# Performance work log

Hardware: AMD Instinct MI355X
Metric: run time of the kernel (lower is better)

## Reference

```python
import jax, jax.numpy as jnp
import numpy as np

H = 2048          # hidden_size
NH = 16           # num heads
DN = 128          # nope_head_dim
DR = 64           # rope_head_dim
DQ = DN + DR      # q_head_dim = 192
DV = 128          # v_head_dim
KVR = 512         # kv_lora_rank
QR = 1536         # q_lora_rank
THETA = 100000.0
EPS = 1e-5


def rms_norm(x, w, eps=EPS):
    var = jnp.mean(x * x, axis=-1, keepdims=True)
    return w * (x * jax.lax.rsqrt(var + eps))


def rotate_half(x):
    x1, x2 = jnp.split(x, 2, axis=-1)
    return jnp.concatenate([-x2, x1], axis=-1)


def rope_cos_sin(seq_len, dim, base, dtype):
    inv_freq = 1.0 / (base ** (jnp.arange(0, dim, 2, dtype=jnp.float32) / dim))
    t = jnp.arange(seq_len, dtype=jnp.float32)
    freqs = jnp.outer(t, inv_freq)          # [S, dim/2]
    emb = jnp.concatenate([freqs, freqs], axis=-1)  # [S, dim]
    return jnp.cos(emb).astype(dtype), jnp.sin(emb).astype(dtype)


def setup_inputs() -> dict:
    key = jax.random.key(0)
    ks = jax.random.split(key, 9)
    B, S = 1, 2048
    sc = lambda fan_in: 1.0 / np.sqrt(fan_in)
    return {
        "x":           jax.random.normal(ks[0], (B, S, H), jnp.float32),
        "wq_down":     jax.random.normal(ks[1], (H, QR), jnp.float32) * sc(H),
        "q_up_norm_w": jnp.ones((QR,), jnp.float32),
        "wq_up":       jax.random.normal(ks[2], (QR, NH * DQ), jnp.float32) * sc(QR),
        "wkv_down":    jax.random.normal(ks[3], (H, KVR), jnp.float32) * sc(H),
        "kv_norm_w":   jnp.ones((KVR,), jnp.float32),
        "wk_up":       jax.random.normal(ks[4], (KVR, NH * DQ), jnp.float32) * sc(KVR),
        "wv_up":       jax.random.normal(ks[5], (KVR, NH * DV), jnp.float32) * sc(KVR),
        "wo":          jax.random.normal(ks[6], (NH * DV, H), jnp.float32) * sc(NH * DV),
    }


def reference(x, wq_down, q_up_norm_w, wq_up, wkv_down, kv_norm_w, wk_up, wv_up, wo):
    B, S, _ = x.shape
    # low-rank Q path
    q_lat = rms_norm(x @ wq_down, q_up_norm_w)
    q = (q_lat @ wq_up).reshape(B, S, NH, DQ)
    q_nope, q_pe = q[..., :DN], q[..., DN:]
    # low-rank KV path
    kv_lat = rms_norm(x @ wkv_down, kv_norm_w)
    k = (kv_lat @ wk_up).reshape(B, S, NH, DQ)
    v = (kv_lat @ wv_up).reshape(B, S, NH, DV)
    k_nope, k_pe = k[..., :DN], k[..., DN:]
    # partial RoPE on the rope dims ([B,S,NH,DR]; cos/sin broadcast over B,NH)
    cos, sin = rope_cos_sin(S, DR, THETA, x.dtype)
    cos = cos[None, :, None, :]
    sin = sin[None, :, None, :]
    q_pe = q_pe * cos + rotate_half(q_pe) * sin
    k_pe = k_pe * cos + rotate_half(k_pe) * sin
    q = jnp.concatenate([q_nope, q_pe], axis=-1)  # [B,S,NH,DQ]
    k = jnp.concatenate([k_nope, k_pe], axis=-1)
    # causal SDPA, scale = 1/sqrt(q_head_dim)
    scale = 1.0 / np.sqrt(DQ)
    scores = jnp.einsum("bqhd,bkhd->bhqk", q, k) * scale
    causal = jnp.tril(jnp.ones((S, S), dtype=bool))
    scores = jnp.where(causal[None, None], scores, jnp.finfo(scores.dtype).min)
    probs = jax.nn.softmax(scores, axis=-1)
    out = jnp.einsum("bhqk,bkhd->bqhd", probs, v).reshape(B, S, NH * DV)
    return out @ wo
```

## Files before the change

kernel.cpp:

```cpp
#include <hip/hip_runtime.h>
#include <math.h>

typedef unsigned short u16;
typedef short s16x8 __attribute__((ext_vector_type(8)));
typedef __bf16 bf16x8 __attribute__((ext_vector_type(8)));
typedef float f32x4 __attribute__((ext_vector_type(4)));

#define S_LEN 2048
#define NHEAD 16
#define QCOLS 3072
#define VCOLS 2048
#define ATT_SCALE 0.07216878364870323f

__device__ __forceinline__ u16 f2bf(float f) {
    unsigned u = __float_as_uint(f);
    u += 0x7fffu + ((u >> 16) & 1u);
    return (u16)(u >> 16);
}
__device__ __forceinline__ float bf2f(u16 h) {
    return __uint_as_float(((unsigned)h) << 16);
}

typedef const __attribute__((address_space(1))) void gas_void;
typedef __attribute__((address_space(3))) void las_void;
__device__ __forceinline__ void gload_lds16(const void* g, void* l) {
    __builtin_amdgcn_global_load_lds(
        (gas_void*)(unsigned long long)g,
        (las_void*)(unsigned)(unsigned long long)l, 16, 0, 0);
}

template<int BM, int BN, int OMODE>
__global__ __launch_bounds__(256) void gemm_bf16(
    const u16* __restrict__ A, const u16* __restrict__ Bt,
    void* __restrict__ Cv, int M, int N, int K,
    const float* __restrict__ cost, const float* __restrict__ sint)
{
    constexpr int BK = 64;
    __shared__ u16 As[2][BM * BK];
    __shared__ u16 Bs[2][BN * BK];
    const int t = threadIdx.x;
    const int lane = t & 63, wid = t >> 6;
    const int wr = wid >> 1, wc = wid & 1;
    const int g = lane >> 4, cl = lane & 15;
    const size_t bm = (size_t)blockIdx.y * BM;
    const size_t bn = (size_t)blockIdx.x * BN;
    constexpr int MR = BM / 32, NR = BN / 32;
    constexpr int APW = BM * BK * 2 / 1024 / 4;
    constexpr int BPW = BN * BK * 2 / 1024 / 4;

    auto stage = [&](int buf, int k0) {
#pragma unroll
        for (int i = 0; i < APW; ++i) {
            int rnd = wid * APW + i;
            int fb  = (rnd << 10) + (lane << 4);
            int row = fb >> 7;
            int ke  = (fb & 127) >> 1;
            gload_lds16(A + (bm + row) * K + k0 + ke, (char*)As[buf] + (rnd << 10));
        }
#pragma unroll
        for (int i = 0; i < BPW; ++i) {
            int rnd = wid * BPW + i;
            int fb  = (rnd << 10) + (lane << 4);
            int row = fb >> 7;
            int ke  = (fb & 127) >> 1;
            gload_lds16(Bt + (bn + row) * K + k0 + ke, (char*)Bs[buf] + (rnd << 10));
        }
    };

    f32x4 acc[MR][NR] = {};
    stage(0, 0);
    int cur = 0;
    for (int k0 = 0; k0 < K; k0 += BK) {
        __syncthreads();
        if (k0 + BK < K) stage(cur ^ 1, k0 + BK);
#pragma unroll
        for (int ks = 0; ks < 2; ++ks) {
            s16x8 av[MR], bv[NR];
#pragma unroll
            for (int m = 0; m < MR; ++m)
                av[m] = *(const s16x8*)((const char*)As[cur] +
                        (wr*(BM/2) + m*16 + cl) * 128 + ks*64 + g*16);
#pragma unroll
            for (int n = 0; n < NR; ++n)
                bv[n] = *(const s16x8*)((const char*)Bs[cur] +
                        (wc*(BN/2) + n*16 + cl) * 128 + ks*64 + g*16);
#pragma unroll
            for (int m = 0; m < MR; ++m)
#pragma unroll
                for (int n = 0; n < NR; ++n)
                    acc[m][n] = __builtin_amdgcn_mfma_f32_16x16x32_bf16(
                        __builtin_bit_cast(bf16x8, av[m]),
                        __builtin_bit_cast(bf16x8, bv[n]), acc[m][n], 0, 0, 0);
        }
        cur ^= 1;
    }

    if constexpr (OMODE == 3) {
        const int band = ((int)(bn >> 6)) + wc;
        const bool pe = (band % 3) == 2;
        u16* C = (u16*)Cv;
#pragma unroll
        for (int m = 0; m < MR; ++m) {
            const size_t rbase = bm + wr*(BM/2) + m*16 + g*4;
            if (pe) {
#pragma unroll
                for (int n = 0; n < 2; ++n) {
                    const int j = n*16 + cl;
                    const size_t colA = bn + wc*(BN/2) + n*16 + cl;
#pragma unroll
                    for (int jj = 0; jj < 4; ++jj) {
                        const size_t r = rbase + jj;
                        float co = cost[r*32 + j], sn = sint[r*32 + j];
                        float a = acc[m][n][jj], b = acc[m][n+2][jj];
                        C[r*N + colA]      = f2bf(a*co - b*sn);
                        C[r*N + colA + 32] = f2bf(b*co + a*sn);
                    }
                }
            } else {
#pragma unroll
                for (int n = 0; n < NR; ++n) {
                    const size_t col = bn + wc*(BN/2) + n*16 + cl;
#pragma unroll
                    for (int jj = 0; jj < 4; ++jj)
                        C[(rbase + jj)*N + col] = f2bf(acc[m][n][jj]);
                }
            }
        }
    } else {
#pragma unroll
        for (int m = 0; m < MR; ++m)
#pragma unroll
            for (int n = 0; n < NR; ++n) {
                size_t col = bn + wc*(BN/2) + n*16 + cl;
#pragma unroll
                for (int j = 0; j < 4; ++j) {
                    size_t row = bm + wr*(BM/2) + m*16 + g*4 + j;
                    if constexpr (OMODE == 0)
                        ((float*)Cv)[row * N + col] = acc[m][n][j];
                    else if constexpr (OMODE == 1)
                        ((u16*)Cv)[row * N + col] = f2bf(acc[m][n][j]);
                    else
                        ((u16*)Cv)[col * M + row] = f2bf(acc[m][n][j]);
                }
            }
    }
}

__global__ __launch_bounds__(256) void transpose_cast5(
    const float* __restrict__ w0, u16* __restrict__ o0,
    const float* __restrict__ w1, u16* __restrict__ o1,
    const float* __restrict__ w2, u16* __restrict__ o2,
    const float* __restrict__ w3, u16* __restrict__ o3,
    const float* __restrict__ w4, u16* __restrict__ o4)
{
    const int z = blockIdx.z;
    const float* in; u16* out; int K, N;
    if      (z == 0) { in = w0; out = o0; K = 2048; N = 1536; }
    else if (z == 1) { in = w1; out = o1; K = 2048; N = 512;  }
    else if (z == 2) { in = w2; out = o2; K = 1536; N = 3072; }
    else if (z == 3) { in = w3; out = o3; K = 512;  N = 3072; }
    else             { in = w4; out = o4; K = 512;  N = 2048; }
    const int bn = blockIdx.x * 32, bk = blockIdx.y * 32;
    if (bn >= N || bk >= K) return;

    __shared__ float tile[32][33];
    const int tx = threadIdx.x & 31, ty = threadIdx.x >> 5;
#pragma unroll
    for (int r = 0; r < 32; r += 8)
        tile[ty + r][tx] = in[(size_t)(bk + ty + r) * N + bn + tx];
    __syncthreads();
#pragma unroll
    for (int r = 0; r < 32; r += 8)
        out[(size_t)(bn + ty + r) * K + bk + tx] = f2bf(tile[tx][ty + r]);
}

__global__ __launch_bounds__(256) void transpose_cast(
    const float* __restrict__ in, u16* __restrict__ out, int K, int N)
{
    __shared__ float tile[32][33];
    const int bk = blockIdx.y * 32, bn = blockIdx.x * 32;
    const int tx = threadIdx.x & 31, ty = threadIdx.x >> 5;
#pragma unroll
    for (int r = 0; r < 32; r += 8)
        tile[ty + r][tx] = in[(size_t)(bk + ty + r) * N + bn + tx];
    __syncthreads();
#pragma unroll
    for (int r = 0; r < 32; r += 8)
        out[(size_t)(bn + ty + r) * K + bk + tx] = f2bf(tile[tx][ty + r]);
}

__global__ __launch_bounds__(256) void cast_f32_bf16(
    const float* __restrict__ in, u16* __restrict__ out, long n)
{
    long i = ((long)blockIdx.x * 256 + threadIdx.x) * 4;
    if (i >= n) return;
    f32x4 v = *(const f32x4*)(in + i);
    ushort4 q;
    q.x = f2bf(v[0]); q.y = f2bf(v[1]); q.z = f2bf(v[2]); q.w = f2bf(v[3]);
    *(ushort4*)(out + i) = q;
}

__global__ __launch_bounds__(256) void rmsnorm_bf(
    const float* __restrict__ x, const float* __restrict__ w,
    u16* __restrict__ o, int N, float invN)
{
    const int row = blockIdx.x;
    const float* xr = x + (size_t)row * N;
    u16* orow = o + (size_t)row * N;
    const int t = threadIdx.x;
    float ss = 0.f;
    for (int i = t * 4; i < N; i += 1024) {
        f32x4 v = *(const f32x4*)&xr[i];
        ss += v[0]*v[0] + v[1]*v[1] + v[2]*v[2] + v[3]*v[3];
    }
#pragma unroll
    for (int off = 32; off > 0; off >>= 1) ss += __shfl_down(ss, off, 64);
    __shared__ float red[4];
    __shared__ float sinv;
    if ((t & 63) == 0) red[t >> 6] = ss;
    __syncthreads();
    if (t == 0) sinv = rsqrtf((red[0]+red[1]+red[2]+red[3]) * invN + 1e-5f);
    __syncthreads();
    const float si = sinv;
    for (int i = t * 4; i < N; i += 1024) {
        f32x4 v = *(const f32x4*)&xr[i];
        f32x4 wv = *(const f32x4*)&w[i];
        ushort4 q;
        q.x = f2bf(v[0]*wv[0]*si); q.y = f2bf(v[1]*wv[1]*si);
        q.z = f2bf(v[2]*wv[2]*si); q.w = f2bf(v[3]*wv[3]*si);
        *(ushort4*)&orow[i] = q;
    }
}

__global__ __launch_bounds__(256) void rope_table_k(
    float* __restrict__ cost, float* __restrict__ sint)
{
    int idx = blockIdx.x * 256 + threadIdx.x;
    int tp = idx >> 5, j = idx & 31;
    float invf = powf(100000.0f, -(float)j * (1.0f / 32.0f));
    float fr = (float)tp * invf;
    cost[idx] = cosf(fr);
    sint[idx] = sinf(fr);
}

__global__ __launch_bounds__(256) void attn_mfma(
    const u16* __restrict__ qg, const u16* __restrict__ kg,
    const u16* __restrict__ vtg, u16* __restrict__ og)
{
    __shared__ u16 Ks[64 * 192];
    __shared__ u16 VTs[128 * 64];
    __shared__ u16 Ps[4][16 * 64];

    const int t = threadIdx.x, lane = t & 63, wid = t >> 6;
    const int g = lane >> 4, cl = lane & 15;
    const int h = blockIdx.y;
    const int bx = blockIdx.x;
    const int qt = (bx & 1) ? (31 - (bx >> 1)) : (bx >> 1);
    const int qbase = qt * 64;
    const int wrow = wid * 16;

    s16x8 qv[6];
    {
        const u16* qrow = qg + (size_t)(qbase + wrow + cl) * QCOLS + h * 192;
#pragma unroll
        for (int s = 0; s < 6; ++s)
            qv[s] = *(const s16x8*)(qrow + s * 32 + g * 8);
    }
    float mreg[4], lreg[4];
#pragma unroll
    for (int j = 0; j < 4; ++j) { mreg[j] = -1e30f; lreg[j] = 0.f; }

    f32x4 accO[8] = {};
    char* pw = (char*)Ps[wid];

    for (int kt = 0; kt <= qt; ++kt) {
        const int kbase = kt * 64;
        __syncthreads();
        {
            const char* ksrc = (const char*)(kg + (size_t)kbase * QCOLS + h * 192);
#pragma unroll
            for (int i = 0; i < 6; ++i) {
                int rnd = wid * 6 + i;
                int fb  = (rnd << 10) + (lane << 4);
                int row = fb / 384;
                int cb  = fb - row * 384;
                gload_lds16(ksrc + (size_t)row * (QCOLS * 2)
                                 + (cb ^ ((row & 7) << 4)),
                            (char*)Ks + (rnd << 10));
            }
            const char* vsrc = (const char*)(vtg + (size_t)(h * 128) * S_LEN + kbase);
#pragma unroll
            for (int i = 0; i < 4; ++i) {
                int rnd = wid * 4 + i;
                int fb  = (rnd << 10) + (lane << 4);
                int dv  = fb >> 7;
                int cb  = fb & 127;
                gload_lds16(vsrc + (size_t)dv * (S_LEN * 2)
                                 + (cb ^ ((dv & 7) << 4)),
                            (char*)VTs + (rnd << 10));
            }
        }
        __syncthreads();

        f32x4 accS[4] = {};
        __builtin_amdgcn_s_setprio(1);
#pragma unroll
        for (int n = 0; n < 4; ++n) {
            const int kvrow = n * 16 + cl;
            const char* krow = (const char*)Ks + kvrow * 384;
            const int sw = (kvrow & 7) << 4;
#pragma unroll
            for (int s = 0; s < 6; ++s) {
                s16x8 kv8 = *(const s16x8*)(krow + ((s * 64 + g * 16) ^ sw));
                accS[n] = __builtin_amdgcn_mfma_f32_16x16x32_bf16(
                    __builtin_bit_cast(bf16x8, qv[s]),
                    __builtin_bit_cast(bf16x8, kv8), accS[n], 0, 0, 0);
            }
        }
        __builtin_amdgcn_s_setprio(0);

        float pm[4][4];
        float cj[4];
#pragma unroll
        for (int j = 0; j < 4; ++j) {
            const int qrow = qbase + wrow + g * 4 + j;
            float mx = -1e30f;
#pragma unroll
            for (int n = 0; n < 4; ++n) {
                int kcol = kbase + n * 16 + cl;
                float s = accS[n][j] * ATT_SCALE;
                s = (kcol <= qrow) ? s : -1e30f;
                pm[n][j] = s;
                mx = fmaxf(mx, s);
            }
#pragma unroll
            for (int off = 1; off < 16; off <<= 1)
                mx = fmaxf(mx, __shfl_xor(mx, off, 64));
            float mnew = fmaxf(mreg[j], mx);
            float c = __expf(mreg[j] - mnew);
            float rs = 0.f;
#pragma unroll
            for (int n = 0; n < 4; ++n) {
                float p = __expf(pm[n][j] - mnew);
                pm[n][j] = p;
                rs += p;
            }
#pragma unroll
            for (int off = 1; off < 16; off <<= 1)
                rs += __shfl_xor(rs, off, 64);
            lreg[j] = lreg[j] * c + rs;
            mreg[j] = mnew;
            cj[j] = c;
        }

#pragma unroll
        for (int n = 0; n < 4; ++n)
#pragma unroll
            for (int j = 0; j < 4; ++j) {
                int q = g * 4 + j;
                int byte = (q * 128 + (n * 16 + cl) * 2) ^ ((q & 7) << 4);
                *(u16*)(pw + byte) = f2bf(pm[n][j]);
            }

#pragma unroll
        for (int nb = 0; nb < 8; ++nb)
#pragma unroll
            for (int j = 0; j < 4; ++j) accO[nb][j] *= cj[j];

        __builtin_amdgcn_s_setprio(1);
#pragma unroll
        for (int ks = 0; ks < 2; ++ks) {
            s16x8 pa = *(const s16x8*)(pw +
                ((cl * 128 + ks * 64 + g * 16) ^ ((cl & 7) << 4)));
#pragma unroll
            for (int nb = 0; nb < 8; ++nb) {
                s16x8 vb = *(const s16x8*)((const char*)VTs +
                    (((nb * 16 + cl) * 128 + ks * 64 + g * 16) ^ ((cl & 7) << 4)));
                accO[nb] = __builtin_amdgcn_mfma_f32_16x16x32_bf16(
                    __builtin_bit_cast(bf16x8, pa),
                    __builtin_bit_cast(bf16x8, vb), accO[nb], 0, 0, 0);
            }
        }
        __builtin_amdgcn_s_setprio(0);
    }

#pragma unroll
    for (int j = 0; j < 4; ++j) {
        float inv = 1.f / lreg[j];
        u16* orow = og + (size_t)(qbase + wrow + g * 4 + j) * VCOLS + h * 128;
#pragma unroll
        for (int nb = 0; nb < 8; ++nb)
            orow[nb * 16 + cl] = f2bf(accO[nb][j] * inv);
    }
}

extern "C" void kernel_launch(void* const* d_in, const int* in_sizes, int n_in,
                              void* d_out, int out_size, void* d_ws, size_t ws_size,
                              hipStream_t stream)
{
    const float* x         = (const float*)d_in[0];
    const float* wq_down   = (const float*)d_in[1];
    const float* q_norm_w  = (const float*)d_in[2];
    const float* wq_up     = (const float*)d_in[3];
    const float* wkv_down  = (const float*)d_in[4];
    const float* kv_norm_w = (const float*)d_in[5];
    const float* wk_up     = (const float*)d_in[6];
    const float* wv_up     = (const float*)d_in[7];
    const float* wo        = (const float*)d_in[8];
    float* out = (float*)d_out;
    char* ws = (char*)d_ws;

    u16*  WQD_T  = (u16*)(ws + 0);
    u16*  WKVD_T = (u16*)(ws + 6291456);
    u16*  WQU_T  = (u16*)(ws + 8388608);
    u16*  WKU_T  = (u16*)(ws + 17825792);
    u16*  WVU_T  = (u16*)(ws + 20971520);
    u16*  XBF    = (u16*)(ws + 23068672);
    float* QLAT  = (float*)(ws + 31457280);
    float* KVLAT = (float*)(ws + 44040192);
    u16*  QLATB  = (u16*)(ws + 48234496);
    u16*  KVLATB = (u16*)(ws + 54525952);
    u16*  QBUF   = (u16*)(ws + 56623104);
    u16*  KBUF   = (u16*)(ws + 69206016);
    float* COST  = (float*)(ws + 81788928);
    float* SINT  = (float*)(ws + 82051072);
    u16*  WO_T   = (u16*)(ws + 0);
    u16*  VTBUF  = (u16*)(ws + 31457280);
    u16*  ATTNO  = (u16*)(ws + 23068672);

    transpose_cast5<<<dim3(96, 64, 5), 256, 0, stream>>>(
        wq_down, WQD_T, wkv_down, WKVD_T, wq_up, WQU_T, wk_up, WKU_T, wv_up, WVU_T);
    cast_f32_bf16<<<4096, 256, 0, stream>>>(x, XBF, (long)S_LEN * 2048);
    rope_table_k<<<256, 256, 0, stream>>>(COST, SINT);

    gemm_bf16<128,128,0><<<dim3(12, 16), 256, 0, stream>>>(
        XBF, WQD_T,  QLAT,  2048, 1536, 2048, nullptr, nullptr);
    gemm_bf16< 64, 64,0><<<dim3( 8, 32), 256, 0, stream>>>(
        XBF, WKVD_T, KVLAT, 2048,  512, 2048, nullptr, nullptr);
    rmsnorm_bf<<<2048, 256, 0, stream>>>(QLAT,  q_norm_w,  QLATB,  1536, 1.f/1536.f);
    rmsnorm_bf<<<2048, 256, 0, stream>>>(KVLAT, kv_norm_w, KVLATB, 512,  1.f/512.f);
    transpose_cast<<<dim3(64, 64), 256, 0, stream>>>(wo, WO_T, 2048, 2048);

    gemm_bf16<128,128,3><<<dim3(24, 16), 256, 0, stream>>>(
        QLATB,  WQU_T, QBUF,  2048, 3072, 1536, COST, SINT);
    gemm_bf16<128,128,3><<<dim3(24, 16), 256, 0, stream>>>(
        KVLATB, WKU_T, KBUF,  2048, 3072, 512,  COST, SINT);
    gemm_bf16<128,128,2><<<dim3(16, 16), 256, 0, stream>>>(
        KVLATB, WVU_T, VTBUF, 2048, 2048, 512,  nullptr, nullptr);

    attn_mfma<<<dim3(32, 16), 256, 0, stream>>>(QBUF, KBUF, VTBUF, ATTNO);
    gemm_bf16<128,128,0><<<dim3(16, 16), 256, 0, stream>>>(
        ATTNO, WO_T, out, 2048, 2048, 2048, nullptr, nullptr);
}
```

Baseline: 375.2 us.

## Fuse K/V up-projections, bf16 latent rmsnorm, register-prefetched attention K/V

The down-projection GEMMs now write bf16 latents directly, and a single combined rmsnorm kernel normalizes both buffers in place. This replaces the fp32 intermediates and the two separate norm launches. The K and V up-projections merge into one GEMM over a contiguous WKU/WVU weight block with N=5120, and blocks past column 3072 write V transposed. The attention kernel swaps the async global-to-LDS loads for register prefetch of the next K/V tile, overlapped with compute. It also transposes the score MFMA so each lane owns one query row, which simplifies the softmax reductions, at the cost of extra syncs and register pressure plus bf16 rounding of the latents before the norm.

```diff
diff --git a/kernel.cpp b/kernel.cpp
--- a/kernel.cpp
+++ b/kernel.cpp
@@ -2,6 +2,7 @@
 #include <math.h>
 
 typedef unsigned short u16;
+typedef short s16x4 __attribute__((ext_vector_type(4)));
 typedef short s16x8 __attribute__((ext_vector_type(8)));
 typedef __bf16 bf16x8 __attribute__((ext_vector_type(8)));
 typedef float f32x4 __attribute__((ext_vector_type(4)));
@@ -33,7 +34,8 @@
 __global__ __launch_bounds__(256) void gemm_bf16(
     const u16* __restrict__ A, const u16* __restrict__ Bt,
     void* __restrict__ Cv, int M, int N, int K,
-    const float* __restrict__ cost, const float* __restrict__ sint)
+    const float* __restrict__ cost, const float* __restrict__ sint,
+    u16* __restrict__ Cv2)
 {
     constexpr int BK = 64;
     __shared__ u16 As[2][BM * BK];
@@ -95,34 +97,49 @@
         cur ^= 1;
     }
 
-    if constexpr (OMODE == 3) {
+    if constexpr (OMODE == 3 || OMODE == 4) {
         const int band = ((int)(bn >> 6)) + wc;
-        const bool pe = (band % 3) == 2;
         u16* C = (u16*)Cv;
-#pragma unroll
-        for (int m = 0; m < MR; ++m) {
-            const size_t rbase = bm + wr*(BM/2) + m*16 + g*4;
-            if (pe) {
-#pragma unroll
-                for (int n = 0; n < 2; ++n) {
-                    const int j = n*16 + cl;
-                    const size_t colA = bn + wc*(BN/2) + n*16 + cl;
-#pragma unroll
-                    for (int jj = 0; jj < 4; ++jj) {
-                        const size_t r = rbase + jj;
-                        float co = cost[r*32 + j], sn = sint[r*32 + j];
-                        float a = acc[m][n][jj], b = acc[m][n+2][jj];
-                        C[r*N + colA]      = f2bf(a*co - b*sn);
-                        C[r*N + colA + 32] = f2bf(b*co + a*sn);
+        if (OMODE == 4 && band >= 48) {
+#pragma unroll
+            for (int m = 0; m < MR; ++m)
+#pragma unroll
+                for (int n = 0; n < NR; ++n) {
+                    size_t vcol = bn + wc*(BN/2) + n*16 + cl - 3072;
+#pragma unroll
+                    for (int j = 0; j < 4; ++j) {
+                        size_t row = bm + wr*(BM/2) + m*16 + g*4 + j;
+                        Cv2[vcol * M + row] = f2bf(acc[m][n][j]);
                     }
                 }
-            } else {
-#pragma unroll
-                for (int n = 0; n < NR; ++n) {
-                    const size_t col = bn + wc*(BN/2) + n*16 + cl;
-#pragma unroll
-                    for (int jj = 0; jj < 4; ++jj)
-                        C[(rbase + jj)*N + col] = f2bf(acc[m][n][jj]);
+        } else {
+            const bool pe = (band % 3) == 2;
+            const int NN = 3072;
+#pragma unroll
+            for (int m = 0; m < MR; ++m) {
+                const size_t rbase = bm + wr*(BM/2) + m*16 + g*4;
+                if (pe) {
+#pragma unroll
+                    for (int n = 0; n < 2; ++n) {
+                        const int j = n*16 + cl;
+                        const size_t colA = bn + wc*(BN/2) + n*16 + cl;
+#pragma unroll
+                        for (int jj = 0; jj < 4; ++jj) {
+                            const size_t r = rbase + jj;
+                            float co = cost[r*32 + j], sn = sint[r*32 + j];
+                            float a = acc[m][n][jj], b = acc[m][n+2][jj];
+                            C[r*NN + colA]      = f2bf(a*co - b*sn);
+                            C[r*NN + colA + 32] = f2bf(b*co + a*sn);
+                        }
+                    }
+                } else {
+#pragma unroll
+                    for (int n = 0; n < NR; ++n) {
+                        const size_t col = bn + wc*(BN/2) + n*16 + cl;
+#pragma unroll
+                        for (int jj = 0; jj < 4; ++jj)
+                            C[(rbase + jj)*NN + col] = f2bf(acc[m][n][jj]);
+                    }
                 }
             }
         }
@@ -200,18 +217,21 @@
     *(ushort4*)(out + i) = q;
 }
 
-__global__ __launch_bounds__(256) void rmsnorm_bf(
-    const float* __restrict__ x, const float* __restrict__ w,
-    u16* __restrict__ o, int N, float invN)
-{
-    const int row = blockIdx.x;
-    const float* xr = x + (size_t)row * N;
-    u16* orow = o + (size_t)row * N;
+__global__ __launch_bounds__(256) void rmsnorm2(
+    u16* __restrict__ qb, const float* __restrict__ qw,
+    u16* __restrict__ kvb, const float* __restrict__ kvw)
+{
+    const int r = blockIdx.x;
+    u16* buf; const float* w; int N; float invN;
+    if (r < 2048) { buf = qb + (size_t)r * 1536; w = qw; N = 1536; invN = 1.f/1536.f; }
+    else { buf = kvb + (size_t)(r - 2048) * 512; w = kvw; N = 512; invN = 1.f/512.f; }
     const int t = threadIdx.x;
+
     float ss = 0.f;
-    for (int i = t * 4; i < N; i += 1024) {
-        f32x4 v = *(const f32x4*)&xr[i];
-        ss += v[0]*v[0] + v[1]*v[1] + v[2]*v[2] + v[3]*v[3];
+    for (int i = t * 8; i < N; i += 2048) {
+        s16x8 v = *(const s16x8*)&buf[i];
+#pragma unroll
+        for (int e = 0; e < 8; ++e) { float f = bf2f((u16)v[e]); ss += f * f; }
     }
 #pragma unroll
     for (int off = 32; off > 0; off >>= 1) ss += __shfl_down(ss, off, 64);
@@ -222,13 +242,13 @@
     if (t == 0) sinv = rsqrtf((red[0]+red[1]+red[2]+red[3]) * invN + 1e-5f);
     __syncthreads();
     const float si = sinv;
-    for (int i = t * 4; i < N; i += 1024) {
-        f32x4 v = *(const f32x4*)&xr[i];
-        f32x4 wv = *(const f32x4*)&w[i];
-        ushort4 q;
-        q.x = f2bf(v[0]*wv[0]*si); q.y = f2bf(v[1]*wv[1]*si);
-        q.z = f2bf(v[2]*wv[2]*si); q.w = f2bf(v[3]*wv[3]*si);
-        *(ushort4*)&orow[i] = q;
+    for (int i = t * 8; i < N; i += 2048) {
+        s16x8 v = *(const s16x8*)&buf[i];
+        s16x8 o;
+#pragma unroll
+        for (int e = 0; e < 8; ++e)
+            o[e] = (short)f2bf(bf2f((u16)v[e]) * w[i + e] * si);
+        *(s16x8*)&buf[i] = o;
     }
 }
 
@@ -266,41 +286,53 @@
         for (int s = 0; s < 6; ++s)
             qv[s] = *(const s16x8*)(qrow + s * 32 + g * 8);
     }
-    float mreg[4], lreg[4];
-#pragma unroll
-    for (int j = 0; j < 4; ++j) { mreg[j] = -1e30f; lreg[j] = 0.f; }
-
+
+    float mreg = -1e30f, lreg = 0.f;
     f32x4 accO[8] = {};
     char* pw = (char*)Ps[wid];
 
+    s16x8 kreg[6], vreg[4];
+    const char* kh = (const char*)(kg + (size_t)h * 192);
+    const char* vh = (const char*)(vtg + (size_t)(h * 128) * S_LEN);
+
+    auto loadKV = [&](int kt2) {
+        const char* ksrc = kh + (size_t)(kt2 * 64) * (QCOLS * 2);
+#pragma unroll
+        for (int i = 0; i < 6; ++i) {
+            int fb = i * 4096 + t * 16;
+            int row = fb / 384, cb = fb - row * 384;
+            kreg[i] = *(const s16x8*)(ksrc + (size_t)row * (QCOLS * 2) + cb);
+        }
+        const char* vsrc = vh + (size_t)(kt2 * 64) * 2;
+#pragma unroll
+        for (int i = 0; i < 4; ++i) {
+            int fb = i * 4096 + t * 16;
+            int dv = fb >> 7, cb = fb & 127;
+            vreg[i] = *(const s16x8*)(vsrc + (size_t)dv * (S_LEN * 2) + cb);
+        }
+    };
+    auto writeKV = [&]() {
+#pragma unroll
+        for (int i = 0; i < 6; ++i) {
+            int fb = i * 4096 + t * 16;
+            int row = fb / 384, cb = fb - row * 384;
+            *(s16x8*)((char*)Ks + row * 384 + (cb ^ ((row & 7) << 4))) = kreg[i];
+        }
+#pragma unroll
+        for (int i = 0; i < 4; ++i) {
+            int fb = i * 4096 + t * 16;
+            int dv = fb >> 7, cb = fb & 127;
+            *(s16x8*)((char*)VTs + dv * 128 + (cb ^ ((dv & 7) << 4))) = vreg[i];
+        }
+    };
+
+    loadKV(0);
+    writeKV();
+    __syncthreads();
+
     for (int kt = 0; kt <= qt; ++kt) {
         const int kbase = kt * 64;
-        __syncthreads();
-        {
-            const char* ksrc = (const char*)(kg + (size_t)kbase * QCOLS + h * 192);
-#pragma unroll
-            for (int i = 0; i < 6; ++i) {
-                int rnd = wid * 6 + i;
-                int fb  = (rnd << 10) + (lane << 4);
-                int row = fb / 384;
-                int cb  = fb - row * 384;
-                gload_lds16(ksrc + (size_t)row * (QCOLS * 2)
-                                 + (cb ^ ((row & 7) << 4)),
-                            (char*)Ks + (rnd << 10));
-            }
-            const char* vsrc = (const char*)(vtg + (size_t)(h * 128) * S_LEN + kbase);
-#pragma unroll
-            for (int i = 0; i < 4; ++i) {
-                int rnd = wid * 4 + i;
-                int fb  = (rnd << 10) + (lane << 4);
-                int dv  = fb >> 7;
-                int cb  = fb & 127;
-                gload_lds16(vsrc + (size_t)dv * (S_LEN * 2)
-                                 + (cb ^ ((dv & 7) << 4)),
-                            (char*)VTs + (rnd << 10));
-            }
-        }
-        __syncthreads();
+        if (kt < qt) loadKV(kt + 1);
 
         f32x4 accS[4] = {};
         __builtin_amdgcn_s_setprio(1);
@@ -313,55 +345,55 @@
             for (int s = 0; s < 6; ++s) {
                 s16x8 kv8 = *(const s16x8*)(krow + ((s * 64 + g * 16) ^ sw));
                 accS[n] = __builtin_amdgcn_mfma_f32_16x16x32_bf16(
-                    __builtin_bit_cast(bf16x8, qv[s]),
-                    __builtin_bit_cast(bf16x8, kv8), accS[n], 0, 0, 0);
+                    __builtin_bit_cast(bf16x8, kv8),
+                    __builtin_bit_cast(bf16x8, qv[s]), accS[n], 0, 0, 0);
             }
         }
         __builtin_amdgcn_s_setprio(0);
 
+        const int qrow_g = qbase + wrow + cl;
         float pm[4][4];
-        float cj[4];
-#pragma unroll
-        for (int j = 0; j < 4; ++j) {
-            const int qrow = qbase + wrow + g * 4 + j;
-            float mx = -1e30f;
-#pragma unroll
-            for (int n = 0; n < 4; ++n) {
-                int kcol = kbase + n * 16 + cl;
+        float mx = -1e30f;
+#pragma unroll
+        for (int n = 0; n < 4; ++n)
+#pragma unroll
+            for (int j = 0; j < 4; ++j) {
+                int kcol = kbase + n * 16 + g * 4 + j;
                 float s = accS[n][j] * ATT_SCALE;
-                s = (kcol <= qrow) ? s : -1e30f;
+                s = (kcol <= qrow_g) ? s : -1e30f;
                 pm[n][j] = s;
                 mx = fmaxf(mx, s);
             }
-#pragma unroll
-            for (int off = 1; off < 16; off <<= 1)
-                mx = fmaxf(mx, __shfl_xor(mx, off, 64));
-            float mnew = fmaxf(mreg[j], mx);
-            float c = __expf(mreg[j] - mnew);
-            float rs = 0.f;
-#pragma unroll
-            for (int n = 0; n < 4; ++n) {
+        mx = fmaxf(mx, __shfl_xor(mx, 16, 64));
+        mx = fmaxf(mx, __shfl_xor(mx, 32, 64));
+        float mnew = fmaxf(mreg, mx);
+        float c = __expf(mreg - mnew);
+        float rs = 0.f;
+#pragma unroll
+        for (int n = 0; n < 4; ++n)
+#pragma unroll
+            for (int j = 0; j < 4; ++j) {
                 float p = __expf(pm[n][j] - mnew);
                 pm[n][j] = p;
                 rs += p;
             }
-#pragma unroll
-            for (int off = 1; off < 16; off <<= 1)
-                rs += __shfl_xor(rs, off, 64);
-            lreg[j] = lreg[j] * c + rs;
-            mreg[j] = mnew;
-            cj[j] = c;
-        }
-
-#pragma unroll
-        for (int n = 0; n < 4; ++n)
-#pragma unroll
-            for (int j = 0; j < 4; ++j) {
-                int q = g * 4 + j;
-                int byte = (q * 128 + (n * 16 + cl) * 2) ^ ((q & 7) << 4);
-                *(u16*)(pw + byte) = f2bf(pm[n][j]);
-            }
-
+        rs += __shfl_xor(rs, 16, 64);
+        rs += __shfl_xor(rs, 32, 64);
+        lreg = lreg * c + rs;
+        mreg = mnew;
+
+#pragma unroll
+        for (int n = 0; n < 4; ++n) {
+            s16x4 pk;
+#pragma unroll
+            for (int j = 0; j < 4; ++j) pk[j] = (short)f2bf(pm[n][j]);
+            int byte = (cl * 128 + n * 32 + g * 8) ^ ((cl & 7) << 4);
+            *(s16x4*)(pw + byte) = pk;
+        }
+
+        float cj[4];
+#pragma unroll
+        for (int j = 0; j < 4; ++j) cj[j] = __shfl(c, g * 4 + j, 64);
 #pragma unroll
         for (int nb = 0; nb < 8; ++nb)
 #pragma unroll
@@ -382,15 +414,21 @@
             }
         }
         __builtin_amdgcn_s_setprio(0);
-    }
-
+
+        __syncthreads();
+        if (kt < qt) writeKV();
+        __syncthreads();
+    }
+
+    float li[4];
+#pragma unroll
+    for (int j = 0; j < 4; ++j) li[j] = 1.f / __shfl(lreg, g * 4 + j, 64);
 #pragma unroll
     for (int j = 0; j < 4; ++j) {
-        float inv = 1.f / lreg[j];
         u16* orow = og + (size_t)(qbase + wrow + g * 4 + j) * VCOLS + h * 128;
 #pragma unroll
         for (int nb = 0; nb < 8; ++nb)
-            orow[nb * 16 + cl] = f2bf(accO[nb][j] * inv);
+            orow[nb * 16 + cl] = f2bf(accO[nb][j] * li[j]);
     }
 }
 
@@ -412,12 +450,11 @@
 
     u16*  WQD_T  = (u16*)(ws + 0);
     u16*  WKVD_T = (u16*)(ws + 6291456);
-    u16*  WQU_T  = (u16*)(ws + 8388608);
-    u16*  WKU_T  = (u16*)(ws + 17825792);
-    u16*  WVU_T  = (u16*)(ws + 20971520);
+    u16*  WKU_T  = (u16*)(ws + 8388608);
+    u16*  WVU_T  = (u16*)(ws + 11534336);
+    u16*  WQU_T  = (u16*)(ws + 13631488);
     u16*  XBF    = (u16*)(ws + 23068672);
-    float* QLAT  = (float*)(ws + 31457280);
-    float* KVLAT = (float*)(ws + 44040192);
+    u16*  VTBUF  = (u16*)(ws + 31457280);
     u16*  QLATB  = (u16*)(ws + 48234496);
     u16*  KVLATB = (u16*)(ws + 54525952);
     u16*  QBUF   = (u16*)(ws + 56623104);
@@ -425,7 +462,6 @@
     float* COST  = (float*)(ws + 81788928);
     float* SINT  = (float*)(ws + 82051072);
     u16*  WO_T   = (u16*)(ws + 0);
-    u16*  VTBUF  = (u16*)(ws + 31457280);
     u16*  ATTNO  = (u16*)(ws + 23068672);
 
     transpose_cast5<<<dim3(96, 64, 5), 256, 0, stream>>>(
@@ -433,22 +469,19 @@
     cast_f32_bf16<<<4096, 256, 0, stream>>>(x, XBF, (long)S_LEN * 2048);
     rope_table_k<<<256, 256, 0, stream>>>(COST, SINT);
 
-    gemm_bf16<128,128,0><<<dim3(12, 16), 256, 0, stream>>>(
-        XBF, WQD_T,  QLAT,  2048, 1536, 2048, nullptr, nullptr);
-    gemm_bf16< 64, 64,0><<<dim3( 8, 32), 256, 0, stream>>>(
-        XBF, WKVD_T, KVLAT, 2048,  512, 2048, nullptr, nullptr);
-    rmsnorm_bf<<<2048, 256, 0, stream>>>(QLAT,  q_norm_w,  QLATB,  1536, 1.f/1536.f);
-    rmsnorm_bf<<<2048, 256, 0, stream>>>(KVLAT, kv_norm_w, KVLATB, 512,  1.f/512.f);
+    gemm_bf16<128,128,1><<<dim3(12, 16), 256, 0, stream>>>(
+        XBF, WQD_T,  QLATB,  2048, 1536, 2048, nullptr, nullptr, nullptr);
+    gemm_bf16< 64, 64,1><<<dim3( 8, 32), 256, 0, stream>>>(
+        XBF, WKVD_T, KVLATB, 2048,  512, 2048, nullptr, nullptr, nullptr);
+    rmsnorm2<<<4096, 256, 0, stream>>>(QLATB, q_norm_w, KVLATB, kv_norm_w);
     transpose_cast<<<dim3(64, 64), 256, 0, stream>>>(wo, WO_T, 2048, 2048);
 
     gemm_bf16<128,128,3><<<dim3(24, 16), 256, 0, stream>>>(
-        QLATB,  WQU_T, QBUF,  2048, 3072, 1536, COST, SINT);
-    gemm_bf16<128,128,3><<<dim3(24, 16), 256, 0, stream>>>(
-        KVLATB, WKU_T, KBUF,  2048, 3072, 512,  COST, SINT);
-    gemm_bf16<128,128,2><<<dim3(16, 16), 256, 0, stream>>>(
-        KVLATB, WVU_T, VTBUF, 2048, 2048, 512,  nullptr, nullptr);
+        QLATB,  WQU_T, QBUF, 2048, 3072, 1536, COST, SINT, nullptr);
+    gemm_bf16<128,128,4><<<dim3(40, 16), 256, 0, stream>>>(
+        KVLATB, WKU_T, KBUF, 2048, 5120, 512,  COST, SINT, VTBUF);
 
     attn_mfma<<<dim3(32, 16), 256, 0, stream>>>(QBUF, KBUF, VTBUF, ATTNO);
     gemm_bf16<128,128,0><<<dim3(16, 16), 256, 0, stream>>>(
-        ATTNO, WO_T, out, 2048, 2048, 2048, nullptr, nullptr);
-}
+        ATTNO, WO_T, out, 2048, 2048, 2048, nullptr, nullptr, nullptr);
+}
```

Measured after the change: 411.6 us. 1.1x slower.
